# Performance work log

Hardware: AMD Instinct MI355X
Metric: run time of the kernel (lower is better)

## Reference

```python
import jax, jax.numpy as jnp
import numpy as np

NUM_LODS = 16
MIN_RES, MAX_RES = 16, 512
CODEBOOK = 1 << 12  # codebook_bitwidth=12
GROWTH = (MAX_RES / MIN_RES) ** (1.0 / (NUM_LODS - 1))
RES = [int(np.floor(MIN_RES * GROWTH ** l)) for l in range(NUM_LODS)]
PRIME_Y = np.uint32(2654435761)  # instant-ngp style spatial hash prime
N_POINTS = 4194304


def setup_inputs() -> dict:
    key = jax.random.key(0)
    ks = jax.random.split(key, 6)
    x = jax.random.uniform(ks[0], (N_POINTS, 2), dtype=jnp.float32)  # coords in [0,1]^2
    latents = 0.1 * jax.random.normal(ks[1], (NUM_LODS, CODEBOOK, 1), dtype=jnp.float32)
    dec_w = 0.1 * jax.random.normal(ks[2], (1, 1), dtype=jnp.float32)  # latent->feature decoder ('sq')
    dec_b = jnp.zeros((1,), dtype=jnp.float32)                          # use_shift=True
    w1 = jax.random.normal(ks[3], (16, 16), dtype=jnp.float32) / 4.0    # hidden_dim=16
    b1 = jnp.zeros((16,), dtype=jnp.float32)
    w2 = jax.random.normal(ks[4], (16, 3), dtype=jnp.float32) / 4.0     # RGB head
    b2 = jnp.zeros((3,), dtype=jnp.float32)
    return {"x": x, "latents": latents, "dec_w": dec_w, "dec_b": dec_b,
            "w1": w1, "b1": b1, "w2": w2, "b2": b2}


def _corner_index(ix, iy, res):
    # dense storage when the grid fits in the codebook, hashed otherwise
    if res * res <= CODEBOOK:
        return ix * res + iy
    h = ix.astype(jnp.uint32) ^ (iy.astype(jnp.uint32) * PRIME_Y)
    return (h % np.uint32(CODEBOOK)).astype(jnp.int32)


def _interp_lod(coords, table, res):
    # coords [N,2] in [0,1]; table [CODEBOOK, F] decoded features for this LOD
    pos = coords * (res - 1)
    p0 = jnp.floor(pos)
    frac = pos - p0
    i0 = p0.astype(jnp.int32)
    i1 = jnp.minimum(i0 + 1, res - 1)
    fx, fy = frac[:, 0:1], frac[:, 1:2]
    f00 = table[_corner_index(i0[:, 0], i0[:, 1], res)]
    f01 = table[_corner_index(i0[:, 0], i1[:, 1], res)]
    f10 = table[_corner_index(i1[:, 0], i0[:, 1], res)]
    f11 = table[_corner_index(i1[:, 0], i1[:, 1], res)]
    return (f00 * (1 - fx) * (1 - fy) + f01 * (1 - fx) * fy
            + f10 * fx * (1 - fy) + f11 * fx * fy)


def reference(x, latents, dec_w, dec_b, w1, b1, w2, b2):
    # Codebook latent decode: decode the (tiny) latent tables once, then gather.
    feat_tables = jnp.einsum('lcd,df->lcf', latents, dec_w) + dec_b  # [L, C, 1]
    feats = [_interp_lod(x, feat_tables[l], RES[l]) for l in range(NUM_LODS)]
    h = jnp.concatenate(feats, axis=-1)  # [N, 16]  (multiscale_type='cat')
    h = jax.nn.relu(h @ w1 + b1)
    return h @ w2 + b2                    # [N, 3] RGB
```

## Files before the change

### kernel.cpp

```cpp
#include <hip/hip_runtime.h>
#include <hip/hip_fp16.h>
#include <math.h>

#define CODEBOOK 4096
#define TPB 1024
#define NWAVES (TPB / 64)
#define CHUNKS 16
#define PTS_PER_BLOCK (TPB * CHUNKS)
#define N_QUAD 4
#define N_PAIR 3
#define N_DENSE 7
#define N_HASH 9
#define QMAX 2305
#define PMAX 8196
#define PRIME 2654435761u

#if defined(__has_builtin)
#if __has_builtin(__builtin_amdgcn_mfma_f32_16x16x16f16)
#define HAVE_MFMA16 1
#endif
#endif
#ifndef HAVE_MFMA16
#define HAVE_MFMA16 0
#endif

typedef _Float16 half4v __attribute__((ext_vector_type(4)));
typedef float    float4v __attribute__((ext_vector_type(4)));

struct Params {
    int      res[16];
    float    rm1[16];
    int      q_off[N_QUAD];
    unsigned magic[N_QUAD];
    int      shift[N_QUAD];
    int      p_off[N_PAIR];
};

__device__ __forceinline__ unsigned pack2(float a, float b) {
    return (unsigned)__half_as_ushort(__float2half(a))
         | ((unsigned)__half_as_ushort(__float2half(b)) << 16);
}

__global__ __launch_bounds__(TPB, 4) void shacira_fwd(
    const float* __restrict__ x,
    const float* __restrict__ latents,
    const float* __restrict__ dec_w,
    const float* __restrict__ dec_b,
    const float* __restrict__ w1,
    const float* __restrict__ b1,
    const float* __restrict__ w2,
    const float* __restrict__ b2,
    float* __restrict__ out,
    Params pr)
{
    __shared__ uint2  dq[QMAX];
    __shared__ unsigned dp[PMAX];
    __shared__ __half hl[N_HASH * CODEBOOK];
#if HAVE_MFMA16
    __shared__ __align__(16) unsigned bounce[NWAVES * 512];
#endif

    const int tid = threadIdx.x;
    const float dw = dec_w[0];
    const float db = dec_b[0];

    #pragma unroll
    for (int l = 0; l < N_QUAD; ++l) {
        const int res = pr.res[l];
        const int n = res * res;
        const unsigned M = pr.magic[l];
        const int sh = pr.shift[l];
        const int off = pr.q_off[l];
        const float* lat = latents + l * CODEBOOK;
        for (int e = tid; e < n; e += TPB) {
            int ix = (int)(((unsigned)e * M) >> sh);
            int iy = e - ix * res;
            int ixp = min(ix + 1, res - 1);
            int iyp = min(iy + 1, res - 1);
            const float* r0 = lat + ix * res;
            const float* r1 = lat + ixp * res;
            uint2 qv;
            qv.x = pack2(fmaf(r0[iy],  dw, db), fmaf(r1[iy],  dw, db));
            qv.y = pack2(fmaf(r0[iyp], dw, db), fmaf(r1[iyp], dw, db));
            dq[off + e] = qv;
        }
    }
    #pragma unroll
    for (int l = 0; l < N_PAIR; ++l) {
        const int res = pr.res[4 + l];
        const int n = res * res;
        const int off = pr.p_off[l];
        const float* lat = latents + (4 + l) * CODEBOOK;
        for (int e = tid; e < n; e += TPB) {
            float a = fmaf(lat[e],     dw, db);
            float b = fmaf(lat[e + 1], dw, db);
            dp[off + e] = pack2(a, b);
        }
    }
    #pragma unroll
    for (int l = 0; l < N_HASH; ++l) {
        const float* lat = latents + (N_DENSE + l) * CODEBOOK;
        for (int e = tid; e < CODEBOOK; e += TPB)
            hl[l * CODEBOOK + e] = __float2half(fmaf(lat[e], dw, db));
    }
    __syncthreads();

    const int lane = tid & 63;
    const int wid  = tid >> 6;
    const int q    = lane >> 4;
    const int r15  = lane & 15;

#if HAVE_MFMA16
    half4v a1f, a2f;
    float4v c1f, c2f;
    #pragma unroll
    for (int j = 0; j < 4; ++j) {
        const int k = q * 4 + j;
        a1f[j] = (_Float16)w1[k * 16 + r15];
        a2f[j] = (r15 < 3) ? (_Float16)w2[k * 3 + r15] : (_Float16)0.f;
        c1f[j] = b1[k];
        c2f[j] = b2[min(k, 2)];
    }
    const int sW = (lane >> 2) & 1;
    const int sR = (r15 >> 2) & 1;
    unsigned* wbase = &bounce[wid * 512 + lane * 8];
#endif

    const int pbase0 = blockIdx.x * PTS_PER_BLOCK;
    const float2* xp = reinterpret_cast<const float2*>(x) + pbase0;
    float* outp = out + (size_t)pbase0 * 3;

    for (int c = 0; c < CHUNKS; ++c) {
        const int t64 = c * TPB + (tid & ~63);
        const float2 xy = xp[t64 + lane];

        float h[16];
        #pragma unroll
        for (int l = 0; l < 16; ++l) {
            const float rm1 = pr.rm1[l];
            const int res = pr.res[l];
            float px = xy.x * rm1, py = xy.y * rm1;
            int i0x = (int)px, i0y = (int)py;
            float fx = __builtin_amdgcn_fractf(px);
            float fy = __builtin_amdgcn_fractf(py);
            if (l < N_QUAD) {
                uint2 qv = dq[pr.q_off[l] + __mul24(i0x, res) + i0y];
                __half2 v0 = *reinterpret_cast<__half2*>(&qv.x);
                __half2 v1 = *reinterpret_cast<__half2*>(&qv.y);
                float f00 = __half2float(__low2half(v0)),  f10 = __half2float(__high2half(v0));
                float f01 = __half2float(__low2half(v1)),  f11 = __half2float(__high2half(v1));
                float a = fmaf(fx, f10 - f00, f00);
                float b = fmaf(fx, f11 - f01, f01);
                h[l] = fmaf(fy, b - a, a);
            } else if (l < N_DENSE) {
                int e = pr.p_off[l - 4] + __mul24(i0x, res) + i0y;
                unsigned u0 = dp[e];
                unsigned u1 = dp[e + ((i0x < res - 1) ? res : 0)];
                __half2 v0 = *reinterpret_cast<__half2*>(&u0);
                __half2 v1 = *reinterpret_cast<__half2*>(&u1);
                float f00 = __half2float(__low2half(v0)),  f01 = __half2float(__high2half(v0));
                float f10 = __half2float(__low2half(v1)),  f11 = __half2float(__high2half(v1));
                float a = fmaf(fy, f01 - f00, f00);
                float b = fmaf(fy, f11 - f10, f10);
                h[l] = fmaf(fx, b - a, a);
            } else {
                int i1x = min(i0x + 1, res - 1);
                int i1y = min(i0y + 1, res - 1);
                unsigned hy0 = (unsigned)i0y * PRIME;
                unsigned hy1 = (i1y == i0y) ? hy0 : hy0 + PRIME;
                const __half* tb = hl + (l - N_DENSE) * CODEBOOK;
                float f00 = __half2float(tb[((unsigned)i0x ^ hy0) & 4095u]);
                float f10 = __half2float(tb[((unsigned)i1x ^ hy0) & 4095u]);
                float f01 = __half2float(tb[((unsigned)i0x ^ hy1) & 4095u]);
                float f11 = __half2float(tb[((unsigned)i1x ^ hy1) & 4095u]);
                float a = fmaf(fy, f01 - f00, f00);
                float b = fmaf(fy, f11 - f10, f10);
                h[l] = fmaf(fx, b - a, a);
            }
        }

#if HAVE_MFMA16
        unsigned hw[8];
        #pragma unroll
        for (int i = 0; i < 8; ++i)
            hw[i] = __builtin_bit_cast(unsigned,
                        __builtin_amdgcn_cvt_pkrtz(h[2 * i], h[2 * i + 1]));
        *reinterpret_cast<uint4*>(wbase + sW * 4)       = uint4{hw[0], hw[1], hw[2], hw[3]};
        *reinterpret_cast<uint4*>(wbase + (sW ^ 1) * 4) = uint4{hw[4], hw[5], hw[6], hw[7]};

        #pragma unroll
        for (int t = 0; t < 4; ++t) {
            const int row = 16 * t + r15;
            const unsigned* rb = &bounce[wid * 512 + row * 8 + ((q * 2) ^ (sR * 4))];
            half4v bf = *reinterpret_cast<const half4v*>(rb);
            float4v d1 = __builtin_amdgcn_mfma_f32_16x16x16f16(a1f, bf, c1f, 0, 0, 0);
            unsigned u0 = __builtin_bit_cast(unsigned,
                              __builtin_amdgcn_cvt_pkrtz(fmaxf(d1[0], 0.f), fmaxf(d1[1], 0.f)));
            unsigned u1 = __builtin_bit_cast(unsigned,
                              __builtin_amdgcn_cvt_pkrtz(fmaxf(d1[2], 0.f), fmaxf(d1[3], 0.f)));
            uint2 uu; uu.x = u0; uu.y = u1;
            half4v rp = __builtin_bit_cast(half4v, uu);
            float4v d2 = __builtin_amdgcn_mfma_f32_16x16x16f16(a2f, rp, c2f, 0, 0, 0);
            if (lane < 16) {
                float* op = outp + (size_t)(t64 + 16 * t + r15) * 3;
                op[0] = d2[0]; op[1] = d2[1]; op[2] = d2[2];
            }
        }
#else
        float o0 = b2[0], o1 = b2[1], o2 = b2[2];
        #pragma unroll
        for (int k = 0; k < 16; ++k) {
            float acc = b1[k];
            #pragma unroll
            for (int l = 0; l < 16; ++l)
                acc = fmaf(h[l], w1[l * 16 + k], acc);
            acc = fmaxf(acc, 0.f);
            o0 = fmaf(acc, w2[k * 3 + 0], o0);
            o1 = fmaf(acc, w2[k * 3 + 1], o1);
            o2 = fmaf(acc, w2[k * 3 + 2], o2);
        }
        float* op = outp + (size_t)(t64 + lane) * 3;
        op[0] = o0; op[1] = o1; op[2] = o2;
#endif
    }
}

extern "C" void kernel_launch(void* const* d_in, const int* in_sizes, int n_in,
                              void* d_out, int out_size, void* d_ws, size_t ws_size,
                              hipStream_t stream)
{
    Params pr;
    const double growth = pow(512.0 / 16.0, 1.0 / 15.0);
    for (int l = 0; l < 16; ++l) {
        pr.res[l] = (int)floor(16.0 * pow(growth, (double)l));
        pr.rm1[l] = (float)(pr.res[l] - 1);
    }
    int qoff = 0;
    for (int l = 0; l < N_QUAD; ++l) {
        pr.q_off[l] = qoff;
        qoff += pr.res[l] * pr.res[l];
        const int d = pr.res[l];
        pr.magic[l] = 0; pr.shift[l] = 0;
        for (int s = 12; s <= 23; ++s) {
            unsigned long long M = ((1ull << s) + d - 1) / d;
            if ((unsigned long long)(d * d - 1) * M >= (1ull << 32)) continue;
            bool ok = true;
            for (int e = 0; e < d * d; ++e)
                if ((int)(((unsigned long long)e * M) >> s) != e / d) { ok = false; break; }
            if (ok) { pr.magic[l] = (unsigned)M; pr.shift[l] = s; break; }
        }
    }
    int poff = 0;
    for (int l = 0; l < N_PAIR; ++l) {
        pr.p_off[l] = poff;
        poff += pr.res[4 + l] * pr.res[4 + l];
    }

    const int n = in_sizes[0] / 2;
    const int blocks = n / PTS_PER_BLOCK;

    shacira_fwd<<<blocks, TPB, 0, stream>>>(
        (const float*)d_in[0], (const float*)d_in[1], (const float*)d_in[2],
        (const float*)d_in[3], (const float*)d_in[4], (const float*)d_in[5],
        (const float*)d_in[6], (const float*)d_in[7], (float*)d_out, pr);
}
```

Baseline: 77.84 us.

## Batch all LDS gathers before interpolation and use 12-bit hash multiply

Restructures the per-point LOD loop so every shared-memory gather for all 16 levels is issued first, separated by scheduling barriers, and the bilinear interpolation runs afterwards. This aims to overlap LDS latency across levels instead of serialising load-then-compute. It also replaces the full 32-bit prime multiply with a 24-bit multiply by the low 12 bits of the prime, which is exact under the 4095 mask, and packs the first-axis lerps as a two-wide FMA. The cost is much higher register pressure from holding raw gathered values for every level, which at 1024 threads per block could cause spills or lower occupancy.

```diff
diff --git a/kernel.cpp b/kernel.cpp
--- a/kernel.cpp
+++ b/kernel.cpp
@@ -14,18 +14,29 @@
 #define QMAX 2305
 #define PMAX 8196
 #define PRIME 2654435761u
+#define PRIME_LO12 0x9B1u
 
 #if defined(__has_builtin)
 #if __has_builtin(__builtin_amdgcn_mfma_f32_16x16x16f16)
 #define HAVE_MFMA16 1
 #endif
+#if __has_builtin(__builtin_amdgcn_sched_barrier)
+#define SBAR() __builtin_amdgcn_sched_barrier(0)
+#endif
+#if __has_builtin(__builtin_elementwise_fma)
+#define HAS_EFMA 1
+#endif
 #endif
 #ifndef HAVE_MFMA16
 #define HAVE_MFMA16 0
 #endif
-
-typedef _Float16 half4v __attribute__((ext_vector_type(4)));
+#ifndef SBAR
+#define SBAR()
+#endif
+
+typedef _Float16 half4v  __attribute__((ext_vector_type(4)));
 typedef float    float4v __attribute__((ext_vector_type(4)));
+typedef float    f32x2   __attribute__((ext_vector_type(2)));
 
 struct Params {
     int      res[16];
@@ -39,6 +50,25 @@
 __device__ __forceinline__ unsigned pack2(float a, float b) {
     return (unsigned)__half_as_ushort(__float2half(a))
          | ((unsigned)__half_as_ushort(__float2half(b)) << 16);
+}
+__device__ __forceinline__ float cvt_lo(unsigned u) {
+    return __half2float(__ushort_as_half((unsigned short)(u & 0xffffu)));
+}
+__device__ __forceinline__ float cvt_hi(unsigned u) {
+    return __half2float(__ushort_as_half((unsigned short)(u >> 16)));
+}
+__device__ __forceinline__ float cvt_us(unsigned short u) {
+    return __half2float(__ushort_as_half(u));
+}
+__device__ __forceinline__ float bilerp(float A0, float A1, float B0, float B1,
+                                        float w, float v) {
+    f32x2 A = {A0, A1}, B = {B0, B1}, W = {w, w};
+#if defined(HAS_EFMA)
+    f32x2 R = __builtin_elementwise_fma(W, B - A, A);
+#else
+    f32x2 R = {fmaf(w, B0 - A0, A0), fmaf(w, B1 - A1, A1)};
+#endif
+    return fmaf(v, R.y - R.x, R.x);
 }
 
 __global__ __launch_bounds__(TPB, 4) void shacira_fwd(
@@ -109,6 +139,7 @@
     const int wid  = tid >> 6;
     const int q    = lane >> 4;
     const int r15  = lane & 15;
+    const unsigned short* hb = reinterpret_cast<const unsigned short*>(hl);
 
 #if HAVE_MFMA16
     half4v a1f, a2f;
@@ -134,49 +165,76 @@
         const int t64 = c * TPB + (tid & ~63);
         const float2 xy = xp[t64 + lane];
 
-        float h[16];
-        #pragma unroll
-        for (int l = 0; l < 16; ++l) {
-            const float rm1 = pr.rm1[l];
+        float fxs[8], fys[8];
+        uint2 qvv[N_QUAD];
+        unsigned pu0[N_PAIR], pu1[N_PAIR];
+        unsigned short h7[4];
+        #pragma unroll
+        for (int l = 0; l < 8; ++l) {
             const int res = pr.res[l];
-            float px = xy.x * rm1, py = xy.y * rm1;
+            float px = xy.x * pr.rm1[l], py = xy.y * pr.rm1[l];
             int i0x = (int)px, i0y = (int)py;
-            float fx = __builtin_amdgcn_fractf(px);
-            float fy = __builtin_amdgcn_fractf(py);
+            fxs[l] = __builtin_amdgcn_fractf(px);
+            fys[l] = __builtin_amdgcn_fractf(py);
             if (l < N_QUAD) {
-                uint2 qv = dq[pr.q_off[l] + __mul24(i0x, res) + i0y];
-                __half2 v0 = *reinterpret_cast<__half2*>(&qv.x);
-                __half2 v1 = *reinterpret_cast<__half2*>(&qv.y);
-                float f00 = __half2float(__low2half(v0)),  f10 = __half2float(__high2half(v0));
-                float f01 = __half2float(__low2half(v1)),  f11 = __half2float(__high2half(v1));
-                float a = fmaf(fx, f10 - f00, f00);
-                float b = fmaf(fx, f11 - f01, f01);
-                h[l] = fmaf(fy, b - a, a);
+                qvv[l] = dq[pr.q_off[l] + (int)__umul24((unsigned)i0x, (unsigned)res) + i0y];
             } else if (l < N_DENSE) {
-                int e = pr.p_off[l - 4] + __mul24(i0x, res) + i0y;
-                unsigned u0 = dp[e];
-                unsigned u1 = dp[e + ((i0x < res - 1) ? res : 0)];
-                __half2 v0 = *reinterpret_cast<__half2*>(&u0);
-                __half2 v1 = *reinterpret_cast<__half2*>(&u1);
-                float f00 = __half2float(__low2half(v0)),  f01 = __half2float(__high2half(v0));
-                float f10 = __half2float(__low2half(v1)),  f11 = __half2float(__high2half(v1));
-                float a = fmaf(fy, f01 - f00, f00);
-                float b = fmaf(fy, f11 - f10, f10);
-                h[l] = fmaf(fx, b - a, a);
+                int e = pr.p_off[l - 4] + (int)__umul24((unsigned)i0x, (unsigned)res) + i0y;
+                pu0[l - 4] = dp[e];
+                pu1[l - 4] = dp[e + ((i0x < res - 1) ? res : 0)];
             } else {
                 int i1x = min(i0x + 1, res - 1);
                 int i1y = min(i0y + 1, res - 1);
-                unsigned hy0 = (unsigned)i0y * PRIME;
-                unsigned hy1 = (i1y == i0y) ? hy0 : hy0 + PRIME;
-                const __half* tb = hl + (l - N_DENSE) * CODEBOOK;
-                float f00 = __half2float(tb[((unsigned)i0x ^ hy0) & 4095u]);
-                float f10 = __half2float(tb[((unsigned)i1x ^ hy0) & 4095u]);
-                float f01 = __half2float(tb[((unsigned)i0x ^ hy1) & 4095u]);
-                float f11 = __half2float(tb[((unsigned)i1x ^ hy1) & 4095u]);
-                float a = fmaf(fy, f01 - f00, f00);
-                float b = fmaf(fy, f11 - f10, f10);
-                h[l] = fmaf(fx, b - a, a);
+                unsigned hy0 = __umul24((unsigned)i0y, PRIME_LO12);
+                unsigned hy1 = (i1y == i0y) ? hy0 : hy0 + PRIME_LO12;
+                h7[0] = hb[((unsigned)i0x ^ hy0) & 4095u];
+                h7[1] = hb[((unsigned)i1x ^ hy0) & 4095u];
+                h7[2] = hb[((unsigned)i0x ^ hy1) & 4095u];
+                h7[3] = hb[((unsigned)i1x ^ hy1) & 4095u];
             }
+        }
+        SBAR();
+
+        unsigned short hv[8][4];
+        #pragma unroll
+        for (int i = 0; i < 8; ++i) {
+            const int l = 8 + i;
+            const int res = pr.res[l];
+            float px = xy.x * pr.rm1[l], py = xy.y * pr.rm1[l];
+            int i0x = (int)px, i0y = (int)py;
+            int i1x = min(i0x + 1, res - 1);
+            int i1y = min(i0y + 1, res - 1);
+            unsigned hy0 = __umul24((unsigned)i0y, PRIME_LO12);
+            unsigned hy1 = (i1y == i0y) ? hy0 : hy0 + PRIME_LO12;
+            const unsigned short* tb = hb + (l - N_DENSE) * CODEBOOK;
+            hv[i][0] = tb[((unsigned)i0x ^ hy0) & 4095u];
+            hv[i][1] = tb[((unsigned)i1x ^ hy0) & 4095u];
+            hv[i][2] = tb[((unsigned)i0x ^ hy1) & 4095u];
+            hv[i][3] = tb[((unsigned)i1x ^ hy1) & 4095u];
+        }
+        SBAR();
+
+        float h[16];
+        #pragma unroll
+        for (int l = 0; l < N_QUAD; ++l) {
+            h[l] = bilerp(cvt_lo(qvv[l].x), cvt_lo(qvv[l].y),
+                          cvt_hi(qvv[l].x), cvt_hi(qvv[l].y), fxs[l], fys[l]);
+        }
+        #pragma unroll
+        for (int l = N_QUAD; l < N_DENSE; ++l) {
+            h[l] = bilerp(cvt_lo(pu0[l - 4]), cvt_lo(pu1[l - 4]),
+                          cvt_hi(pu0[l - 4]), cvt_hi(pu1[l - 4]), fys[l], fxs[l]);
+        }
+        h[7] = bilerp(cvt_us(h7[0]), cvt_us(h7[1]), cvt_us(h7[2]), cvt_us(h7[3]),
+                      fys[7], fxs[7]);
+        #pragma unroll
+        for (int i = 0; i < 8; ++i) {
+            const int l = 8 + i;
+            float px = xy.x * pr.rm1[l], py = xy.y * pr.rm1[l];
+            float fx = __builtin_amdgcn_fractf(px);
+            float fy = __builtin_amdgcn_fractf(py);
+            h[l] = bilerp(cvt_us(hv[i][0]), cvt_us(hv[i][1]),
+                          cvt_us(hv[i][2]), cvt_us(hv[i][3]), fy, fx);
         }
 
 #if HAVE_MFMA16
```

After: 77.75 us. About the same (-0.1%).
